# Optimization experiments

Hardware: AMD Instinct MI355X
Metric: run time of the kernel (lower is better)

## Reference

```python
import jax, jax.numpy as jnp
import numpy as np

D_MODEL = 1024
D_HEAD = 64
N_HEADS = D_MODEL // D_HEAD
MAX_SEQ = 2048
BATCH = 2
SEQ = 2048


def setup_inputs() -> dict:
    key = jax.random.key(0)
    ks = jax.random.split(key, 10)
    s = 1.0 / np.sqrt(D_MODEL)
    return {
        "x": jax.random.normal(ks[0], (BATCH, SEQ, D_MODEL), dtype=jnp.float32),
        "Wq": jax.random.normal(ks[1], (D_MODEL, D_MODEL), dtype=jnp.float32) * s,
        "bq": jax.random.normal(ks[2], (D_MODEL,), dtype=jnp.float32) * 0.01,
        "Wk": jax.random.normal(ks[3], (D_MODEL, D_MODEL), dtype=jnp.float32) * s,
        "bk": jax.random.normal(ks[4], (D_MODEL,), dtype=jnp.float32) * 0.01,
        "Wv": jax.random.normal(ks[5], (D_MODEL, D_MODEL), dtype=jnp.float32) * s,
        "bv": jax.random.normal(ks[6], (D_MODEL,), dtype=jnp.float32) * 0.01,
        "Er": jax.random.normal(ks[7], (MAX_SEQ, D_HEAD), dtype=jnp.float32),
        "Wo": jax.random.normal(ks[8], (D_MODEL, D_MODEL), dtype=jnp.float32) * s,
        "bo": jax.random.normal(ks[9], (D_MODEL,), dtype=jnp.float32) * 0.01,
    }


def _s_rel(q, Er):
    # q: [B,H,S,Dh]; use last S rows of Er (start = max_seq - seq)
    S = q.shape[2]
    Er_slice = Er[Er.shape[0] - S:, :]                  # [S, Dh]
    qE = jnp.einsum("bhsd,ld->bhsl", q, Er_slice)       # [B,H,S,S]
    padded = jnp.pad(qE, ((0, 0), (0, 0), (0, 0), (1, 0)))  # [B,H,S,S+1]
    B, H, S1, S2 = padded.shape
    padded = padded.reshape(B, H, S2, S1)               # skew trick
    return padded[:, :, 1:, :]                          # [B,H,S,S]


def reference(x, Wq, bq, Wk, bk, Wv, bv, Er, Wo, bo):
    B, S, _ = x.shape
    scale = 1.0 / np.sqrt(D_HEAD)
    # projections (torch Linear: x @ W.T + b)
    def proj(W, b):
        return (x @ W.T + b).reshape(B, S, N_HEADS, D_HEAD).transpose(0, 2, 1, 3)
    q = proj(Wq, bq)   # [B,H,S,Dh]
    k = proj(Wk, bk)
    v = proj(Wv, bv)
    qk = jnp.einsum("bhsd,bhtd->bhst", q, k)            # [B,H,S,S]
    logits = (qk + _s_rel(q, Er)) * scale
    causal = jnp.tril(jnp.ones((S, S), dtype=bool))
    masked = jnp.where(causal[None, None], logits, -1e9)
    attn = jax.nn.softmax(masked, axis=-1)
    out = jnp.einsum("bhst,bhtd->bhsd", attn, v)        # [B,H,S,Dh]
    out = out.transpose(0, 2, 1, 3).reshape(B, S, D_MODEL)
    return out @ Wo.T + bo
```

## Files before the change

kernel.cpp:

```cpp
#include <hip/hip_runtime.h>
#include <hip/hip_bf16.h>

typedef short v8s __attribute__((ext_vector_type(8)));
typedef float v4f __attribute__((ext_vector_type(4)));
typedef __hip_bfloat16 bf16;
typedef unsigned int u32;

#define MFMA(a, b, c) __builtin_amdgcn_mfma_f32_16x16x32_bf16(a, b, c, 0, 0, 0)

__device__ __forceinline__ void gload16(const bf16* g, bf16* l) {
    __builtin_amdgcn_global_load_lds(
        (const __attribute__((address_space(1))) u32*)(g),
        (__attribute__((address_space(3))) u32*)(l), 16, 0, 0);
}

__global__ __launch_bounds__(256) void cast_all(
    const float* __restrict__ x,  const float* __restrict__ wq,
    const float* __restrict__ wk, const float* __restrict__ wv,
    const float* __restrict__ wo, const float* __restrict__ er,
    bf16* __restrict__ xb,  bf16* __restrict__ wqb, bf16* __restrict__ wkb,
    bf16* __restrict__ wvb, bf16* __restrict__ wob, bf16* __restrict__ erb)
{
    const int r = blockIdx.y;
    const float* s; bf16* d; int n4;
    if      (r == 0) { s = x;  d = xb;  n4 = 1048576; }
    else if (r == 1) { s = wq; d = wqb; n4 = 262144;  }
    else if (r == 2) { s = wk; d = wkb; n4 = 262144;  }
    else if (r == 3) { s = wv; d = wvb; n4 = 262144;  }
    else if (r == 4) { s = wo; d = wob; n4 = 262144;  }
    else             { s = er; d = erb; n4 = 32768;   }
    const int i = blockIdx.x * 256 + threadIdx.x;
    if (i < n4) {
        const float4 v = ((const float4*)s)[i];
        bf16 t[4];
        t[0] = __float2bfloat16(v.x);
        t[1] = __float2bfloat16(v.y);
        t[2] = __float2bfloat16(v.z);
        t[3] = __float2bfloat16(v.w);
        ((uint2*)d)[i] = *(const uint2*)t;
    }
}

__global__ __launch_bounds__(256) void gemm_nt(
    const bf16* __restrict__ A, const bf16* __restrict__ W,
    const float* __restrict__ b0, const float* __restrict__ b1,
    const float* __restrict__ b2,
    bf16* __restrict__ oHM, bf16* __restrict__ Vt, float* __restrict__ outf)
{
    __shared__ bf16 As[128 * 64];
    __shared__ bf16 Bs[128 * 64];

    const int tid = threadIdx.x;
    const int w  = tid >> 6, l = tid & 63;
    const int lm = l & 15,  lq = l >> 4;
    const int wm = (w >> 1) * 64, wn = (w & 1) * 64;
    const int m0 = blockIdx.y * 128, n0 = blockIdx.x * 128;

    const int grow = l >> 3;
    const int gcol = ((l & 7) ^ grow) * 8;

    v4f acc[4][4];
#pragma unroll
    for (int i = 0; i < 4; ++i)
#pragma unroll
        for (int j = 0; j < 4; ++j) acc[i][j] = (v4f){0.f, 0.f, 0.f, 0.f};

    const int sw = (lm & 7) << 4;

    for (int k0 = 0; k0 < 1024; k0 += 64) {
        __syncthreads();
#pragma unroll
        for (int q = 0; q < 4; ++q) {
            const int rr = w * 32 + q * 8;
            gload16(&A[(size_t)(m0 + rr + grow) * 1024 + k0 + gcol], &As[rr * 64]);
            gload16(&W[(size_t)(n0 + rr + grow) * 1024 + k0 + gcol], &Bs[rr * 64]);
        }
        __syncthreads();
#pragma unroll
        for (int kk = 0; kk < 2; ++kk) {
            v8s a[4], b[4];
            const int cb = (lq * 16 + kk * 64);
#pragma unroll
            for (int i = 0; i < 4; ++i) {
                const int row = wm + i * 16 + lm;
                a[i] = *(const v8s*)((const char*)As + row * 128 + (cb ^ sw));
            }
#pragma unroll
            for (int j = 0; j < 4; ++j) {
                const int row = wn + j * 16 + lm;
                b[j] = *(const v8s*)((const char*)Bs + row * 128 + (cb ^ sw));
            }
#pragma unroll
            for (int i = 0; i < 4; ++i)
#pragma unroll
                for (int j = 0; j < 4; ++j)
                    acc[i][j] = MFMA(b[j], a[i], acc[i][j]);
        }
    }

    const int z = blockIdx.x >> 3;
    const float* bias = (z == 0) ? b0 : (z == 1) ? b1 : b2;

    float4 bj[4];
#pragma unroll
    for (int j = 0; j < 4; ++j)
        bj[j] = *(const float4*)&bias[(n0 & 1023) + wn + j * 16 + lq * 4];

#pragma unroll
    for (int i = 0; i < 4; ++i) {
        const int row = m0 + wm + i * 16 + lm;
        const int bb = row >> 11, ss = row & 2047;
#pragma unroll
        for (int j = 0; j < 4; ++j) {
            const int cc = (n0 & 1023) + wn + j * 16 + lq * 4;
            const float v0 = acc[i][j][0] + bj[j].x;
            const float v1 = acc[i][j][1] + bj[j].y;
            const float v2 = acc[i][j][2] + bj[j].z;
            const float v3 = acc[i][j][3] + bj[j].w;
            if (outf) {
                const float4 fv = {v0, v1, v2, v3};
                *(float4*)&outf[(size_t)row * 1024 + cc] = fv;
            } else {
                bf16 t[4];
                t[0] = __float2bfloat16(v0);
                t[1] = __float2bfloat16(v1);
                t[2] = __float2bfloat16(v2);
                t[3] = __float2bfloat16(v3);
                const int hh = cc >> 6, dd = cc & 63;
                if (z < 2) {
                    *(uint2*)&oHM[(size_t)z * 4194304 +
                        ((size_t)(bb * 16 + hh) * 2048 + ss) * 64 + dd] = *(uint2*)t;
                } else {
#pragma unroll
                    for (int r = 0; r < 4; ++r)
                        Vt[((size_t)(bb * 16 + hh) * 64 + dd + r) * 2048 + ss] = t[r];
                }
            }
        }
    }
}

__global__ __launch_bounds__(256, 4) void attn(
    const bf16* __restrict__ Q, const bf16* __restrict__ K,
    const bf16* __restrict__ Vt, const bf16* __restrict__ Er,
    bf16* __restrict__ AO)
{
    __shared__ bf16 Ks[64 * 72];
    __shared__ bf16 Vs[64 * 72];
    __shared__ bf16 Ps[64 * 72];
    __shared__ bf16 Gs[64 * 84];

    const int ord = blockIdx.x;
    const int u = ord & 255, j = ord >> 8;
    const int a = u & 31, yh = u >> 5;
    const int q1 = (j & 2) ? (a ^ 16) : a;
    const int qb = (j & 1) ? (31 - q1) : q1;
    const int bh = 8 * j + yh;

    const int i0 = qb * 64;
    const int b  = bh >> 4, h = bh & 15;
    const int tid = threadIdx.x;
    const int w  = tid >> 6, l = tid & 63;
    const int lm = l & 15,  lq = l >> 4;

    const bf16* qp = Q + ((size_t)bh * 2048 + i0 + w * 16 + lm) * 64 + lq * 8;
    const v8s q0 = *(const v8s*)qp;
    const v8s q1f = *(const v8s*)(qp + 32);

    v4f accO[4];
#pragma unroll
    for (int dt = 0; dt < 4; ++dt) accO[dt] = (v4f){0.f, 0.f, 0.f, 0.f};
    float rs[4];
#pragma unroll
    for (int r = 0; r < 4; ++r) rs[r] = 0.f;

    const int sr0 = tid >> 3;
    const int sc8 = (tid & 7) * 8;
    const size_t kbase = (size_t)bh * 2048 * 64;
    const size_t vbase = (size_t)bh * 64 * 2048;

    const int nk = qb + 1;

    uint4 kp0 = *(const uint4*)&K[kbase + (size_t)sr0 * 64 + sc8];
    uint4 kp1 = *(const uint4*)&K[kbase + (size_t)(sr0 + 32) * 64 + sc8];
    uint4 vp0 = *(const uint4*)&Vt[vbase + (size_t)sr0 * 2048 + sc8];
    uint4 vp1 = *(const uint4*)&Vt[vbase + (size_t)(sr0 + 32) * 2048 + sc8];

    for (int it = 0; it < nk; ++it) {
        const int j0 = it * 64;
        __syncthreads();
        *(uint4*)&Ks[sr0 * 72 + sc8]        = kp0;
        *(uint4*)&Ks[(sr0 + 32) * 72 + sc8] = kp1;
        *(uint4*)&Vs[sr0 * 72 + sc8]        = vp0;
        *(uint4*)&Vs[(sr0 + 32) * 72 + sc8] = vp1;
        if (it + 1 < nk) {
            const int jn = j0 + 64;
            kp0 = *(const uint4*)&K[kbase + (size_t)(jn + sr0) * 64 + sc8];
            kp1 = *(const uint4*)&K[kbase + (size_t)(jn + sr0 + 32) * 64 + sc8];
            vp0 = *(const uint4*)&Vt[vbase + (size_t)sr0 * 2048 + jn + sc8];
            vp1 = *(const uint4*)&Vt[vbase + (size_t)(sr0 + 32) * 2048 + jn + sc8];
        }
        const int basew = 2048 - 16 - i0 + j0 - 16 * w;
#pragma unroll
        for (int ct2 = 0; ct2 < 5; ++ct2) {
            int mr = basew + ct2 * 16 + lm;
            mr = (mr > 2047) ? 2047 : mr;
            const bf16* ep = Er + (size_t)mr * 64 + lq * 8;
            const v8s e0 = *(const v8s*)ep;
            const v8s e1 = *(const v8s*)(ep + 32);
            v4f g = (v4f){0.f, 0.f, 0.f, 0.f};
            g = MFMA(q0, e0, g);
            g = MFMA(q1f, e1, g);
#pragma unroll
            for (int r = 0; r < 4; ++r)
                Gs[(w * 16 + lq * 4 + r) * 84 + ct2 * 16 + lm] =
                    __float2bfloat16(g[r] * 0.125f);
        }
        __syncthreads();
        v4f sv[4];
#pragma unroll
        for (int ct = 0; ct < 4; ++ct) {
            const v8s k0f = *(const v8s*)&Ks[(ct * 16 + lm) * 72 + lq * 8];
            const v8s k1f = *(const v8s*)&Ks[(ct * 16 + lm) * 72 + 32 + lq * 8];
            v4f s = (v4f){0.f, 0.f, 0.f, 0.f};
            s = MFMA(q0, k0f, s);
            s = MFMA(q1f, k1f, s);
            sv[ct] = s;
        }
#pragma unroll
        for (int r = 0; r < 4; ++r) {
            const int rl = lq * 4 + r;
            const int ig = i0 + w * 16 + rl;
#pragma unroll
            for (int ct = 0; ct < 4; ++ct) {
                const int jj = ct * 16 + lm;
                const float gb = (float)Gs[(w * 16 + rl) * 84 + jj + 15 - rl];
                float s = fmaf(sv[ct][r], 0.125f, gb);
                if (j0 + jj > ig) s = -1e9f;
                const float pe = __expf(s - 4.0f);
                rs[r] += pe;
                Ps[(w * 16 + rl) * 72 + jj] = __float2bfloat16(pe);
            }
        }
        const v8s pa0 = *(const v8s*)&Ps[(w * 16 + lm) * 72 + lq * 8];
        const v8s pa1 = *(const v8s*)&Ps[(w * 16 + lm) * 72 + 32 + lq * 8];
#pragma unroll
        for (int dt = 0; dt < 4; ++dt) {
            const v8s vb0 = *(const v8s*)&Vs[(dt * 16 + lm) * 72 + lq * 8];
            const v8s vb1 = *(const v8s*)&Vs[(dt * 16 + lm) * 72 + 32 + lq * 8];
            accO[dt] = MFMA(vb0, pa0, accO[dt]);
            accO[dt] = MFMA(vb1, pa1, accO[dt]);
        }
    }
#pragma unroll
    for (int r = 0; r < 4; ++r) {
#pragma unroll
        for (int msk = 8; msk >= 1; msk >>= 1)
            rs[r] += __shfl_xor(rs[r], msk, 64);
    }
    const int srcl = (lm >> 2) * 16;
    const float s0 = __shfl(rs[0], srcl, 64);
    const float s1 = __shfl(rs[1], srcl, 64);
    const float s2 = __shfl(rs[2], srcl, 64);
    const float s3 = __shfl(rs[3], srcl, 64);
    const float den = (lm & 2) ? ((lm & 1) ? s3 : s2) : ((lm & 1) ? s1 : s0);
    const float inv = 1.0f / den;
    const int rowo = i0 + w * 16 + lm;
#pragma unroll
    for (int dt = 0; dt < 4; ++dt) {
        bf16 t[4];
#pragma unroll
        for (int r = 0; r < 4; ++r) t[r] = __float2bfloat16(accO[dt][r] * inv);
        *(uint2*)&AO[((size_t)b * 2048 + rowo) * 1024 + h * 64 + dt * 16 + lq * 4] =
            *(uint2*)t;
    }
}

extern "C" void kernel_launch(void* const* d_in, const int* in_sizes, int n_in,
                              void* d_out, int out_size, void* d_ws, size_t ws_size,
                              hipStream_t stream)
{
    const float* x  = (const float*)d_in[0];
    const float* Wq = (const float*)d_in[1];
    const float* bq = (const float*)d_in[2];
    const float* Wk = (const float*)d_in[3];
    const float* bk = (const float*)d_in[4];
    const float* Wv = (const float*)d_in[5];
    const float* bv = (const float*)d_in[6];
    const float* Er = (const float*)d_in[7];
    const float* Wo = (const float*)d_in[8];
    const float* bo = (const float*)d_in[9];
    float* out = (float*)d_out;

    bf16* ws = (bf16*)d_ws;
    const size_t NEl = (size_t)4096 * 1024;
    bf16* Qw  = ws;
    bf16* Kw  = ws + NEl;
    bf16* Vtw = ws + 3 * NEl;
    bf16* xb  = ws + 4 * NEl;
    bf16* AOw = xb;
    bf16* Wqb = ws + 5 * NEl;
    bf16* Wkb = Wqb + 1024 * 1024;
    bf16* Wvb = Wkb + 1024 * 1024;
    bf16* Wob = Wvb + 1024 * 1024;
    bf16* Erb = Wob + 1024 * 1024;
    (void)Kw;

    cast_all<<<dim3(4096, 6), 256, 0, stream>>>(x, Wq, Wk, Wv, Wo, Er,
                                                xb, Wqb, Wkb, Wvb, Wob, Erb);
    gemm_nt<<<dim3(24, 32), 256, 0, stream>>>(xb, Wqb, bq, bk, bv, Qw, Vtw, nullptr);
    attn<<<dim3(1024), 256, 0, stream>>>(Qw, Kw, Vtw, Erb, AOw);
    gemm_nt<<<dim3(8, 32), 256, 0, stream>>>(AOw, Wob, bo, bo, bo, nullptr, nullptr, out);
}
```

Measured before the change: 287.0 us.

## Split long causal attention rows across two blocks with partial-sum fixup

Query blocks 17-31 now have their KV range split in half across two workgroups. Each half writes unnormalized fp32 partial outputs and row sums, and a new fixup kernel adds the two halves and normalizes them; short rows still run in one block. The change also merges the G and P shared buffers to cut LDS use, raises the occupancy hint to 5, and swaps the MFMA operand order for the PV product. The aim is to balance the causal triangle's load across CUs, at the cost of an extra kernel launch and partial traffic staged in the output buffer.

```diff
diff --git a/kernel.cpp b/kernel.cpp
--- a/kernel.cpp
+++ b/kernel.cpp
@@ -140,22 +140,32 @@
     }
 }
 
-__global__ __launch_bounds__(256, 4) void attn(
+__global__ __launch_bounds__(256, 5) void attn(
     const bf16* __restrict__ Q, const bf16* __restrict__ K,
     const bf16* __restrict__ Vt, const bf16* __restrict__ Er,
-    bf16* __restrict__ AO)
+    bf16* __restrict__ AO, float* __restrict__ Opart, float* __restrict__ dpart)
 {
     __shared__ bf16 Ks[64 * 72];
     __shared__ bf16 Vs[64 * 72];
-    __shared__ bf16 Ps[64 * 72];
-    __shared__ bf16 Gs[64 * 84];
+    __shared__ bf16 GPs[64 * 84];
 
     const int ord = blockIdx.x;
-    const int u = ord & 255, j = ord >> 8;
-    const int a = u & 31, yh = u >> 5;
-    const int q1 = (j & 2) ? (a ^ 16) : a;
-    const int qb = (j & 1) ? (31 - q1) : q1;
-    const int bh = 8 * j + yh;
+    int bh, qb, t0, t1, slot = -1;
+    if (ord < 960) {
+        qb = 31 - (ord >> 6);
+        const int sub = ord & 63;
+        bh = sub >> 1;
+        const int half = sub & 1;
+        const int hh2 = (qb + 1) >> 1;
+        t0 = half ? hh2 : 0;
+        t1 = half ? (qb + 1) : hh2;
+        slot = ((31 - qb) * 32 + bh) * 2 + half;
+    } else {
+        const int g2 = ord - 960;
+        qb = 16 - (g2 >> 5);
+        bh = g2 & 31;
+        t0 = 0; t1 = qb + 1;
+    }
 
     const int i0 = qb * 64;
     const int b  = bh >> 4, h = bh & 15;
@@ -179,21 +189,20 @@
     const size_t kbase = (size_t)bh * 2048 * 64;
     const size_t vbase = (size_t)bh * 64 * 2048;
 
-    const int nk = qb + 1;
-
-    uint4 kp0 = *(const uint4*)&K[kbase + (size_t)sr0 * 64 + sc8];
-    uint4 kp1 = *(const uint4*)&K[kbase + (size_t)(sr0 + 32) * 64 + sc8];
-    uint4 vp0 = *(const uint4*)&Vt[vbase + (size_t)sr0 * 2048 + sc8];
-    uint4 vp1 = *(const uint4*)&Vt[vbase + (size_t)(sr0 + 32) * 2048 + sc8];
-
-    for (int it = 0; it < nk; ++it) {
+    const int jt0 = t0 * 64;
+    uint4 kp0 = *(const uint4*)&K[kbase + (size_t)(jt0 + sr0) * 64 + sc8];
+    uint4 kp1 = *(const uint4*)&K[kbase + (size_t)(jt0 + sr0 + 32) * 64 + sc8];
+    uint4 vp0 = *(const uint4*)&Vt[vbase + (size_t)sr0 * 2048 + jt0 + sc8];
+    uint4 vp1 = *(const uint4*)&Vt[vbase + (size_t)(sr0 + 32) * 2048 + jt0 + sc8];
+
+    for (int it = t0; it < t1; ++it) {
         const int j0 = it * 64;
         __syncthreads();
         *(uint4*)&Ks[sr0 * 72 + sc8]        = kp0;
         *(uint4*)&Ks[(sr0 + 32) * 72 + sc8] = kp1;
         *(uint4*)&Vs[sr0 * 72 + sc8]        = vp0;
         *(uint4*)&Vs[(sr0 + 32) * 72 + sc8] = vp1;
-        if (it + 1 < nk) {
+        if (it + 1 < t1) {
             const int jn = j0 + 64;
             kp0 = *(const uint4*)&K[kbase + (size_t)(jn + sr0) * 64 + sc8];
             kp1 = *(const uint4*)&K[kbase + (size_t)(jn + sr0 + 32) * 64 + sc8];
@@ -213,7 +222,7 @@
             g = MFMA(q1f, e1, g);
 #pragma unroll
             for (int r = 0; r < 4; ++r)
-                Gs[(w * 16 + lq * 4 + r) * 84 + ct2 * 16 + lm] =
+                GPs[(w * 16 + lq * 4 + r) * 84 + ct2 * 16 + lm] =
                     __float2bfloat16(g[r] * 0.125f);
         }
         __syncthreads();
@@ -234,22 +243,22 @@
 #pragma unroll
             for (int ct = 0; ct < 4; ++ct) {
                 const int jj = ct * 16 + lm;
-                const float gb = (float)Gs[(w * 16 + rl) * 84 + jj + 15 - rl];
+                const float gb = (float)GPs[(w * 16 + rl) * 84 + jj + 15 - rl];
                 float s = fmaf(sv[ct][r], 0.125f, gb);
                 if (j0 + jj > ig) s = -1e9f;
                 const float pe = __expf(s - 4.0f);
                 rs[r] += pe;
-                Ps[(w * 16 + rl) * 72 + jj] = __float2bfloat16(pe);
-            }
-        }
-        const v8s pa0 = *(const v8s*)&Ps[(w * 16 + lm) * 72 + lq * 8];
-        const v8s pa1 = *(const v8s*)&Ps[(w * 16 + lm) * 72 + 32 + lq * 8];
+                GPs[(w * 16 + rl) * 84 + jj] = __float2bfloat16(pe);
+            }
+        }
+        const v8s pa0 = *(const v8s*)&GPs[(w * 16 + lm) * 84 + lq * 8];
+        const v8s pa1 = *(const v8s*)&GPs[(w * 16 + lm) * 84 + 32 + lq * 8];
 #pragma unroll
         for (int dt = 0; dt < 4; ++dt) {
             const v8s vb0 = *(const v8s*)&Vs[(dt * 16 + lm) * 72 + lq * 8];
             const v8s vb1 = *(const v8s*)&Vs[(dt * 16 + lm) * 72 + 32 + lq * 8];
-            accO[dt] = MFMA(vb0, pa0, accO[dt]);
-            accO[dt] = MFMA(vb1, pa1, accO[dt]);
+            accO[dt] = MFMA(pa0, vb0, accO[dt]);
+            accO[dt] = MFMA(pa1, vb1, accO[dt]);
         }
     }
 #pragma unroll
@@ -258,21 +267,59 @@
         for (int msk = 8; msk >= 1; msk >>= 1)
             rs[r] += __shfl_xor(rs[r], msk, 64);
     }
-    const int srcl = (lm >> 2) * 16;
-    const float s0 = __shfl(rs[0], srcl, 64);
-    const float s1 = __shfl(rs[1], srcl, 64);
-    const float s2 = __shfl(rs[2], srcl, 64);
-    const float s3 = __shfl(rs[3], srcl, 64);
-    const float den = (lm & 2) ? ((lm & 1) ? s3 : s2) : ((lm & 1) ? s1 : s0);
-    const float inv = 1.0f / den;
-    const int rowo = i0 + w * 16 + lm;
-#pragma unroll
-    for (int dt = 0; dt < 4; ++dt) {
-        bf16 t[4];
-#pragma unroll
-        for (int r = 0; r < 4; ++r) t[r] = __float2bfloat16(accO[dt][r] * inv);
-        *(uint2*)&AO[((size_t)b * 2048 + rowo) * 1024 + h * 64 + dt * 16 + lq * 4] =
-            *(uint2*)t;
+    if (slot < 0) {
+#pragma unroll
+        for (int dt = 0; dt < 4; ++dt) {
+#pragma unroll
+            for (int r = 0; r < 4; ++r) {
+                const int row = i0 + w * 16 + lq * 4 + r;
+                const int d   = dt * 16 + lm;
+                const float v = accO[dt][r] / rs[r];
+                AO[((size_t)b * 2048 + row) * 1024 + h * 64 + d] = __float2bfloat16(v);
+            }
+        }
+    } else {
+        float* op = Opart + (size_t)slot * 4096;
+#pragma unroll
+        for (int dt = 0; dt < 4; ++dt) {
+#pragma unroll
+            for (int r = 0; r < 4; ++r) {
+                const int row = w * 16 + lq * 4 + r;
+                op[row * 64 + dt * 16 + lm] = accO[dt][r];
+            }
+        }
+        if (lm == 0) {
+#pragma unroll
+            for (int r = 0; r < 4; ++r)
+                dpart[slot * 64 + w * 16 + lq * 4 + r] = rs[r];
+        }
+    }
+}
+
+__global__ __launch_bounds__(256) void fixup(
+    const float* __restrict__ Opart, const float* __restrict__ dpart,
+    bf16* __restrict__ AO)
+{
+    const int pi = blockIdx.x;
+    const int qb = 31 - (pi >> 5);
+    const int bh = pi & 31;
+    const int b = bh >> 4, h = bh & 15;
+    const int t = threadIdx.x;
+    const int row = t >> 2;
+    const int c0 = (t & 3) * 16;
+    const float dA = dpart[(pi * 2) * 64 + row];
+    const float dB = dpart[(pi * 2 + 1) * 64 + row];
+    const float inv = 1.0f / (dA + dB);
+    const float* A = Opart + (size_t)(pi * 2) * 4096 + row * 64 + c0;
+    const float* B = Opart + (size_t)(pi * 2 + 1) * 4096 + row * 64 + c0;
+    bf16* dst = AO + ((size_t)b * 2048 + qb * 64 + row) * 1024 + h * 64 + c0;
+#pragma unroll
+    for (int c = 0; c < 16; c += 4) {
+        bf16 tt[4];
+#pragma unroll
+        for (int r = 0; r < 4; ++r)
+            tt[r] = __float2bfloat16((A[c + r] + B[c + r]) * inv);
+        *(uint2*)&dst[c] = *(uint2*)tt;
     }
 }
 
@@ -304,11 +351,14 @@
     bf16* Wvb = Wkb + 1024 * 1024;
     bf16* Wob = Wvb + 1024 * 1024;
     bf16* Erb = Wob + 1024 * 1024;
+    float* dpart = (float*)(Erb + (size_t)2048 * 64);
+    float* Opart = out;
     (void)Kw;
 
     cast_all<<<dim3(4096, 6), 256, 0, stream>>>(x, Wq, Wk, Wv, Wo, Er,
                                                 xb, Wqb, Wkb, Wvb, Wob, Erb);
     gemm_nt<<<dim3(24, 32), 256, 0, stream>>>(xb, Wqb, bq, bk, bv, Qw, Vtw, nullptr);
-    attn<<<dim3(1024), 256, 0, stream>>>(Qw, Kw, Vtw, Erb, AOw);
+    attn<<<dim3(1504), 256, 0, stream>>>(Qw, Kw, Vtw, Erb, AOw, Opart, dpart);
+    fixup<<<dim3(480), 256, 0, stream>>>(Opart, dpart, AOw);
     gemm_nt<<<dim3(8, 32), 256, 0, stream>>>(AOw, Wob, bo, bo, bo, nullptr, nullptr, out);
 }
```

New measurement: 328.5 us. 14.5% more time.

## Double-buffer GEMM LDS tiles and transpose PV MFMA output layout

Applied to the files above, without the earlier changes.

The projection GEMM now uses two LDS buffers, issuing the async global-to-LDS loads for the next K tile before computing the current one, with one barrier per iteration instead of two. This is meant to hide global load latency behind MFMA work, at the cost of twice the shared memory, which may lower occupancy. Separately, the attention PV MFMA swaps its operands, so each lane holds rows matching its own row-sum registers. That removes the cross-lane shuffles used to fetch the denominator, but output stores become scalar 2-byte writes instead of 8-byte vector stores.

```diff
diff --git a/kernel.cpp b/kernel.cpp
--- a/kernel.cpp
+++ b/kernel.cpp
@@ -47,8 +47,8 @@
     const float* __restrict__ b2,
     bf16* __restrict__ oHM, bf16* __restrict__ Vt, float* __restrict__ outf)
 {
-    __shared__ bf16 As[128 * 64];
-    __shared__ bf16 Bs[128 * 64];
+    __shared__ bf16 As[2][128 * 64];
+    __shared__ bf16 Bs[2][128 * 64];
 
     const int tid = threadIdx.x;
     const int w  = tid >> 6, l = tid & 63;
@@ -67,15 +67,15 @@
 
     const int sw = (lm & 7) << 4;
 
-    for (int k0 = 0; k0 < 1024; k0 += 64) {
-        __syncthreads();
+    auto STAGE = [&](int p, int k0) {
 #pragma unroll
         for (int q = 0; q < 4; ++q) {
             const int rr = w * 32 + q * 8;
-            gload16(&A[(size_t)(m0 + rr + grow) * 1024 + k0 + gcol], &As[rr * 64]);
-            gload16(&W[(size_t)(n0 + rr + grow) * 1024 + k0 + gcol], &Bs[rr * 64]);
-        }
-        __syncthreads();
+            gload16(&A[(size_t)(m0 + rr + grow) * 1024 + k0 + gcol], &As[p][rr * 64]);
+            gload16(&W[(size_t)(n0 + rr + grow) * 1024 + k0 + gcol], &Bs[p][rr * 64]);
+        }
+    };
+    auto COMPUTE = [&](int p) {
 #pragma unroll
         for (int kk = 0; kk < 2; ++kk) {
             v8s a[4], b[4];
@@ -83,12 +83,12 @@
 #pragma unroll
             for (int i = 0; i < 4; ++i) {
                 const int row = wm + i * 16 + lm;
-                a[i] = *(const v8s*)((const char*)As + row * 128 + (cb ^ sw));
+                a[i] = *(const v8s*)((const char*)As[p] + row * 128 + (cb ^ sw));
             }
 #pragma unroll
             for (int j = 0; j < 4; ++j) {
                 const int row = wn + j * 16 + lm;
-                b[j] = *(const v8s*)((const char*)Bs + row * 128 + (cb ^ sw));
+                b[j] = *(const v8s*)((const char*)Bs[p] + row * 128 + (cb ^ sw));
             }
 #pragma unroll
             for (int i = 0; i < 4; ++i)
@@ -96,7 +96,16 @@
                 for (int j = 0; j < 4; ++j)
                     acc[i][j] = MFMA(b[j], a[i], acc[i][j]);
         }
-    }
+    };
+
+    STAGE(0, 0);
+    __syncthreads();
+    for (int t = 0; t < 15; ++t) {
+        STAGE((t + 1) & 1, (t + 1) * 64);
+        COMPUTE(t & 1);
+        __syncthreads();
+    }
+    COMPUTE(1);
 
     const int z = blockIdx.x >> 3;
     const float* bias = (z == 0) ? b0 : (z == 1) ? b1 : b2;
@@ -248,8 +257,8 @@
         for (int dt = 0; dt < 4; ++dt) {
             const v8s vb0 = *(const v8s*)&Vs[(dt * 16 + lm) * 72 + lq * 8];
             const v8s vb1 = *(const v8s*)&Vs[(dt * 16 + lm) * 72 + 32 + lq * 8];
-            accO[dt] = MFMA(vb0, pa0, accO[dt]);
-            accO[dt] = MFMA(vb1, pa1, accO[dt]);
+            accO[dt] = MFMA(pa0, vb0, accO[dt]);
+            accO[dt] = MFMA(pa1, vb1, accO[dt]);
         }
     }
 #pragma unroll
@@ -258,21 +267,15 @@
         for (int msk = 8; msk >= 1; msk >>= 1)
             rs[r] += __shfl_xor(rs[r], msk, 64);
     }
-    const int srcl = (lm >> 2) * 16;
-    const float s0 = __shfl(rs[0], srcl, 64);
-    const float s1 = __shfl(rs[1], srcl, 64);
-    const float s2 = __shfl(rs[2], srcl, 64);
-    const float s3 = __shfl(rs[3], srcl, 64);
-    const float den = (lm & 2) ? ((lm & 1) ? s3 : s2) : ((lm & 1) ? s1 : s0);
-    const float inv = 1.0f / den;
-    const int rowo = i0 + w * 16 + lm;
 #pragma unroll
     for (int dt = 0; dt < 4; ++dt) {
-        bf16 t[4];
-#pragma unroll
-        for (int r = 0; r < 4; ++r) t[r] = __float2bfloat16(accO[dt][r] * inv);
-        *(uint2*)&AO[((size_t)b * 2048 + rowo) * 1024 + h * 64 + dt * 16 + lq * 4] =
-            *(uint2*)t;
+#pragma unroll
+        for (int r = 0; r < 4; ++r) {
+            const int row = i0 + w * 16 + lq * 4 + r;
+            const int d   = dt * 16 + lm;
+            const float v = accO[dt][r] / rs[r];
+            AO[((size_t)b * 2048 + row) * 1024 + h * 64 + d] = __float2bfloat16(v);
+        }
     }
 }
 
```

Measured after the change: 276.9 us. 3.5% less time.
